# Kernel optimization log

Measured on AMD Instinct MI355X. Metric: run time of the kernel, lower is better.

Reference implementation:

```python
import jax, jax.numpy as jnp
import numpy as np

NUM_HEADS = 4
GN_GROUPS = 32
EPS = 1e-5


def setup_inputs() -> dict:
    key = jax.random.key(0)
    ks = jax.random.split(key, 6)
    B, C, H, W = 4, 256, 64, 64
    return {
        "x": jax.random.normal(ks[0], (B, C, H, W), dtype=jnp.float32),
        "gn_w": jnp.ones((C,), dtype=jnp.float32),
        "gn_b": jnp.zeros((C,), dtype=jnp.float32),
        "qkv_w": jax.random.normal(ks[1], (3 * C, C), dtype=jnp.float32) * 0.05,
        "qkv_b": jax.random.normal(ks[2], (3 * C,), dtype=jnp.float32) * 0.02,
        "proj_w": jax.random.normal(ks[3], (C, C), dtype=jnp.float32) * 0.05,
        "proj_b": jax.random.normal(ks[4], (C,), dtype=jnp.float32) * 0.02,
    }


def reference(x, gn_w, gn_b, qkv_w, qkv_b, proj_w, proj_b):
    b, c, h, w = x.shape
    L = h * w
    xf = x.reshape(b, c, L)

    # GroupNorm32: normalize over (channels_per_group, length) in float32
    xg = xf.reshape(b, GN_GROUPS, (c // GN_GROUPS) * L).astype(jnp.float32)
    mean = xg.mean(axis=-1, keepdims=True)
    var = xg.var(axis=-1, keepdims=True)
    xn = ((xg - mean) * jax.lax.rsqrt(var + EPS)).reshape(b, c, L).astype(x.dtype)
    xn = xn * gn_w[:, None] + gn_b[:, None]

    # 1x1 Conv1d == channel matmul: [3C, C] @ [b, C, L]
    qkv = jnp.einsum('oc,bcl->bol', qkv_w, xn) + qkv_b[:, None]

    # QKVAttentionLegacy
    ch = c // NUM_HEADS
    qkv_h = qkv.reshape(b * NUM_HEADS, 3 * ch, L)
    q, k, v = qkv_h[:, :ch], qkv_h[:, ch:2 * ch], qkv_h[:, 2 * ch:]
    scale = 1.0 / np.sqrt(np.sqrt(ch)).astype(np.float32)
    weight = jnp.einsum('bct,bcs->bts', q * scale, k * scale)  # [b*H, L, L]
    weight = jax.nn.softmax(weight.astype(jnp.float32), axis=-1).astype(qkv.dtype)
    a = jnp.einsum('bts,bcs->bct', weight, v).reshape(b, c, L)

    h_out = jnp.einsum('oc,bcl->bol', proj_w, a) + proj_b[:, None]
    return (xf + h_out).reshape(b, c, h, w)
```

## Files before the change

kernel.cpp:

```cpp
#include <hip/hip_runtime.h>
#include <math.h>

#define L 4096
#define C 256

typedef __attribute__((ext_vector_type(8))) short bf16x8;
typedef __attribute__((ext_vector_type(4))) short s16x4;
typedef __attribute__((ext_vector_type(4))) float f32x4;
typedef __attribute__((ext_vector_type(2))) unsigned int u32x2;
typedef __attribute__((ext_vector_type(4))) unsigned int u32x4;

#define MFMA16(a, b, c) __builtin_amdgcn_mfma_f32_16x16x32_bf16(a, b, c, 0, 0, 0)

static __device__ __forceinline__ short f2bf(float f) {
  union { float f; unsigned u; } x{f};
  unsigned r = (x.u + 0x7fffu + ((x.u >> 16) & 1u)) >> 16;
  return (short)r;
}
static __device__ __forceinline__ unsigned pack2(float a, float b) {
  return (unsigned)(unsigned short)f2bf(a) | ((unsigned)(unsigned short)f2bf(b) << 16);
}
static __device__ __forceinline__ unsigned ppack(float a, float b) {
  union { float f; unsigned u; } xa{a}, xb{b};
  return __builtin_amdgcn_perm(xb.u, xa.u, 0x07060302u);
}
static __device__ __forceinline__ float bflo(unsigned u) {
  union { unsigned u; float f; } x{u << 16};
  return x.f;
}
static __device__ __forceinline__ float bfhi(unsigned u) {
  union { unsigned u; float f; } x{u & 0xffff0000u};
  return x.f;
}
static __device__ __forceinline__ void gload_lds16(const void* g, void* l) {
  __builtin_amdgcn_global_load_lds(
      (const __attribute__((address_space(1))) unsigned int*)g,
      (__attribute__((address_space(3))) unsigned int*)l, 16, 0, 0);
}

__global__ __launch_bounds__(256) void prep(const float* __restrict__ x,
    float* __restrict__ gnp, short* __restrict__ xbf,
    const float* __restrict__ wa, const float* __restrict__ wb,
    short* __restrict__ da, short* __restrict__ db) {
  int blk = blockIdx.x;
  int tid = threadIdx.x;
  if (blk < 512) {
    size_t base = (size_t)blk * 8192;
    const f32x4* xp = (const f32x4*)(x + base);
    u32x2* xo = (u32x2*)(xbf + base);
    float s = 0.f, ss = 0.f;
    #pragma unroll
    for (int i = 0; i < 8; ++i) {
      f32x4 v = xp[i * 256 + tid];
      s  += v[0] + v[1] + v[2] + v[3];
      ss += v[0]*v[0] + v[1]*v[1] + v[2]*v[2] + v[3]*v[3];
      u32x2 o;
      o[0] = pack2(v[0], v[1]);
      o[1] = pack2(v[2], v[3]);
      xo[i * 256 + tid] = o;
    }
    __shared__ float rs[256], rss[256];
    rs[tid] = s; rss[tid] = ss;
    __syncthreads();
    for (int off = 128; off > 0; off >>= 1) {
      if (tid < off) { rs[tid] += rs[tid + off]; rss[tid] += rss[tid + off]; }
      __syncthreads();
    }
    if (tid == 0) {
      gnp[(size_t)blk * 2]     = rs[0];
      gnp[(size_t)blk * 2 + 1] = rss[0];
    }
  } else {
    int i = (blk - 512) * 256 + tid;
    if (i < 768 * C) da[i] = f2bf(wa[i]);
    else db[i - 768 * C] = f2bf(wb[i - 768 * C]);
  }
}

__global__ __launch_bounds__(256) void gn_apply(const short* __restrict__ xbf,
    const float* __restrict__ gw, const float* __restrict__ gb,
    const float* __restrict__ gnp, short* __restrict__ xnT) {
  int bg = blockIdx.y;
  int b = bg >> 5, g = bg & 31;
  int tid = threadIdx.x;
  const short* xg = xbf + (size_t)bg * 32768;

  float s  = gnp[(size_t)(bg*4)*2]   + gnp[(size_t)(bg*4+1)*2] +
             gnp[(size_t)(bg*4+2)*2] + gnp[(size_t)(bg*4+3)*2];
  float ss = gnp[(size_t)(bg*4)*2+1]   + gnp[(size_t)(bg*4+1)*2+1] +
             gnp[(size_t)(bg*4+2)*2+1] + gnp[(size_t)(bg*4+3)*2+1];
  float mean = s * (1.f / 32768.f);
  float var  = ss * (1.f / 32768.f) - mean * mean;
  float rstd = rsqrtf(var + 1e-5f);

  float scl[8], sft[8];
  #pragma unroll
  for (int c = 0; c < 8; ++c) {
    float wv = gw[g * 8 + c], bv = gb[g * 8 + c];
    scl[c] = rstd * wv;
    sft[c] = bv - mean * rstd * wv;
  }

  short* outb = xnT + (size_t)b * L * C + g * 8;
  int lb = blockIdx.x * 1024 + tid * 4;
  u32x2 raw[8];
  #pragma unroll
  for (int c = 0; c < 8; ++c)
    raw[c] = *(const u32x2*)(xg + (size_t)c * L + lb);
  #pragma unroll
  for (int j = 0; j < 4; ++j) {
    u32x4 ov;
    #pragma unroll
    for (int cp = 0; cp < 4; ++cp) {
      unsigned w0 = raw[2 * cp][j >> 1], w1 = raw[2 * cp + 1][j >> 1];
      float a = (j & 1) ? bfhi(w0) : bflo(w0);
      float bb = (j & 1) ? bfhi(w1) : bflo(w1);
      ov[cp] = pack2(a * scl[2 * cp] + sft[2 * cp],
                     bb * scl[2 * cp + 1] + sft[2 * cp + 1]);
    }
    *(u32x4*)(outb + (size_t)(lb + j) * C) = ov;
  }
}

__global__ __launch_bounds__(256) void qkv_mfma(const short* __restrict__ wq,
    const float* __restrict__ bias, const short* __restrict__ xnT,
    short* __restrict__ qT, short* __restrict__ kT, short* __restrict__ vB) {
  int tid = threadIdx.x;
  int wid = tid >> 6, lane = tid & 63, g = lane >> 4, lr = lane & 15;
  int oy = blockIdx.y;
  int o0 = oy * 64;
  int b  = blockIdx.z;
  int head = oy / 3, kind = oy % 3;
  int bh = b * 4 + head;
  int lw = blockIdx.x * 128 + wid * 32;
  const short* xb = xnT + (size_t)b * L * C;

  f32x4 acc[4][2];
  #pragma unroll
  for (int m = 0; m < 4; ++m)
    #pragma unroll
    for (int nt = 0; nt < 2; ++nt) acc[m][nt] = (f32x4)0.f;

  #pragma unroll 2
  for (int k0 = 0; k0 < C; k0 += 32) {
    bf16x8 af[4], bfr[2];
    #pragma unroll
    for (int m = 0; m < 4; ++m)
      af[m] = *(const bf16x8*)(wq + (size_t)(o0 + m * 16 + lr) * C + k0 + g * 8);
    #pragma unroll
    for (int nt = 0; nt < 2; ++nt)
      bfr[nt] = *(const bf16x8*)(xb + (size_t)(lw + nt * 16 + lr) * C + k0 + g * 8);
    #pragma unroll
    for (int m = 0; m < 4; ++m)
      #pragma unroll
      for (int nt = 0; nt < 2; ++nt)
        acc[m][nt] = MFMA16(af[m], bfr[nt], acc[m][nt]);
  }

  float sc = (kind == 0) ? 0.51014930f : (kind == 1) ? 0.35355339f : 1.0f;
  if (kind == 2) {
    #pragma unroll
    for (int m = 0; m < 4; ++m)
      #pragma unroll
      for (int nt = 0; nt < 2; ++nt)
        #pragma unroll
        for (int r = 0; r < 4; ++r) {
          int o = m * 16 + g * 4 + r;
          vB[((size_t)bh * 64 + o) * L + lw + nt * 16 + lr] =
              f2bf(acc[m][nt][r] + bias[o0 + o]);
        }
  } else {
    short* dst = (kind == 0 ? qT : kT);
    #pragma unroll
    for (int m = 0; m < 4; ++m)
      #pragma unroll
      for (int nt = 0; nt < 2; ++nt) {
        s16x4 pk;
        #pragma unroll
        for (int r = 0; r < 4; ++r)
          pk[r] = f2bf((acc[m][nt][r] + bias[o0 + m * 16 + g * 4 + r]) * sc);
        *(s16x4*)(dst + ((size_t)bh * L + lw + nt * 16 + lr) * 64 + m * 16 + g * 4) = pk;
      }
  }
}

__global__ __launch_bounds__(512) void attn_mfma(
    const short* __restrict__ qT, const short* __restrict__ kT,
    const short* __restrict__ vB, short* __restrict__ amatT) {
  int orig = blockIdx.x;
  int bid = (orig & 7) * 32 + (orig >> 3);
  int bh = bid >> 4, qb = bid & 15;
  int b = bh >> 2, h = bh & 3;
  int tid = threadIdx.x;
  int wid = tid >> 6, lane = tid & 63;
  int g = lane >> 4, lr = lane & 15;
  int tw = qb * 256 + wid * 32;
  int lx7 = lr & 7;
  int pswA = ((lr & 3) << 4) | ((lr >> 2) << 2);

  const short* qTh = qT + (size_t)bh * L * 64;
  const short* kTh = kT + (size_t)bh * L * 64;
  const short* vh  = vB + (size_t)bh * 64 * L;

  __shared__ short Kt[4][64 * 64];
  __shared__ short Vt[4][64 * 64];
  __shared__ short plds[8][32][64];

  bf16x8 qf[2][2];
  #pragma unroll
  for (int nt = 0; nt < 2; ++nt)
    #pragma unroll
    for (int ks = 0; ks < 2; ++ks)
      qf[nt][ks] = *(const bf16x8*)(qTh + (size_t)(tw + nt * 16 + lr) * 64 +
                                    ks * 32 + g * 8);

  bf16x8 ones;
  #pragma unroll
  for (int i = 0; i < 8; ++i) ones[i] = (short)0x3F80;

  f32x4 acc[4][2], acc_l[2];
  #pragma unroll
  for (int cm = 0; cm < 4; ++cm)
    #pragma unroll
    for (int nt = 0; nt < 2; ++nt) acc[cm][nt] = (f32x4)0.f;
  acc_l[0] = (f32x4)0.f; acc_l[1] = (f32x4)0.f;

  size_t koff, voff;
  int ldsc;
  {
    int r = tid >> 3, c16 = tid & 7;
    int cs = c16 ^ (r & 7);
    koff = (size_t)r * 64 + cs * 8;
    voff = (size_t)r * L + cs * 8;
    ldsc = wid * 512;
  }

  gload_lds16(kTh + koff, &Kt[0][ldsc]);
  gload_lds16(vh + voff, &Vt[0][ldsc]);
  gload_lds16(kTh + koff + (size_t)64 * 64, &Kt[1][ldsc]);
  gload_lds16(vh + voff + 64, &Vt[1][ldsc]);

  int sl = 0;
  #pragma unroll 1
  for (int s = 0; s < 32; ++s) {
    if (s < 31) {
      int nb = sl ^ 2;
      size_t t0 = (size_t)(2 * s + 2) * 64, t1 = (size_t)(2 * s + 3) * 64;
      gload_lds16(kTh + koff + t0 * 64, &Kt[nb][ldsc]);
      gload_lds16(vh + voff + t0, &Vt[nb][ldsc]);
      gload_lds16(kTh + koff + t1 * 64, &Kt[nb + 1][ldsc]);
      gload_lds16(vh + voff + t1, &Vt[nb + 1][ldsc]);
      asm volatile("s_waitcnt vmcnt(4)" ::: "memory");
    } else {
      asm volatile("s_waitcnt vmcnt(0)" ::: "memory");
    }
    __builtin_amdgcn_sched_barrier(0);
    __builtin_amdgcn_s_barrier();

    const short* Ka = &Kt[sl][0];     const short* Va = &Vt[sl][0];
    const short* Kb = &Kt[sl + 1][0]; const short* Vb = &Vt[sl + 1][0];

    f32x4 st0[4][2], st1[4][2];
    __builtin_amdgcn_s_setprio(1);
    #pragma unroll
    for (int sm = 0; sm < 4; ++sm) {
      int row = sm * 16 + lr;
      bf16x8 kf0 = *(const bf16x8*)&Ka[row * 64 + ((g ^ lx7)) * 8];
      bf16x8 kf1 = *(const bf16x8*)&Ka[row * 64 + (((4 + g) ^ lx7)) * 8];
      #pragma unroll
      for (int nt = 0; nt < 2; ++nt) {
        f32x4 cc = (f32x4)0.f;
        cc = MFMA16(kf0, qf[nt][0], cc);
        cc = MFMA16(kf1, qf[nt][1], cc);
        st0[sm][nt] = cc;
      }
    }
    __builtin_amdgcn_s_setprio(0);
    #pragma unroll
    for (int sm = 0; sm < 4; ++sm) {
      int row = sm * 16 + lr;
      bf16x8 kf0 = *(const bf16x8*)&Kb[row * 64 + ((g ^ lx7)) * 8];
      bf16x8 kf1 = *(const bf16x8*)&Kb[row * 64 + (((4 + g) ^ lx7)) * 8];
      #pragma unroll
      for (int nt = 0; nt < 2; ++nt) {
        f32x4 cc = (f32x4)0.f;
        cc = MFMA16(kf0, qf[nt][0], cc);
        cc = MFMA16(kf1, qf[nt][1], cc);
        st1[sm][nt] = cc;
        u32x2 w;
        w[0] = ppack(__builtin_amdgcn_exp2f(st0[sm][nt][0]),
                     __builtin_amdgcn_exp2f(st0[sm][nt][1]));
        w[1] = ppack(__builtin_amdgcn_exp2f(st0[sm][nt][2]),
                     __builtin_amdgcn_exp2f(st0[sm][nt][3]));
        *(u32x2*)&plds[wid][nt * 16 + lr][(sm * 16 + g * 4) ^ pswA] = w;
      }
    }
    bf16x8 pf0[2][2];
    #pragma unroll
    for (int nt = 0; nt < 2; ++nt)
      #pragma unroll
      for (int ks = 0; ks < 2; ++ks) {
        s16x4 pa = *(const s16x4*)&plds[wid][nt * 16 + lr][(ks * 32 + g * 8) ^ pswA];
        s16x4 pb = *(const s16x4*)&plds[wid][nt * 16 + lr][(ks * 32 + g * 8 + 4) ^ pswA];
        pf0[nt][ks] = __builtin_shufflevector(pa, pb, 0, 1, 2, 3, 4, 5, 6, 7);
      }
    #pragma unroll
    for (int nt = 0; nt < 2; ++nt) {
      acc_l[nt] = MFMA16(ones, pf0[nt][0], acc_l[nt]);
      acc_l[nt] = MFMA16(ones, pf0[nt][1], acc_l[nt]);
    }
    #pragma unroll
    for (int cm = 0; cm < 4; ++cm) {
      int row = cm * 16 + lr;
      bf16x8 vf0 = *(const bf16x8*)&Va[row * 64 + ((g ^ lx7)) * 8];
      bf16x8 vf1 = *(const bf16x8*)&Va[row * 64 + (((4 + g) ^ lx7)) * 8];
      #pragma unroll
      for (int nt = 0; nt < 2; ++nt) {
        acc[cm][nt] = MFMA16(vf0, pf0[nt][0], acc[cm][nt]);
        acc[cm][nt] = MFMA16(vf1, pf0[nt][1], acc[cm][nt]);
        u32x2 w;
        w[0] = ppack(__builtin_amdgcn_exp2f(st1[cm][nt][0]),
                     __builtin_amdgcn_exp2f(st1[cm][nt][1]));
        w[1] = ppack(__builtin_amdgcn_exp2f(st1[cm][nt][2]),
                     __builtin_amdgcn_exp2f(st1[cm][nt][3]));
        *(u32x2*)&plds[wid][nt * 16 + lr][(cm * 16 + g * 4) ^ pswA] = w;
      }
    }
    bf16x8 pf1[2][2];
    #pragma unroll
    for (int nt = 0; nt < 2; ++nt)
      #pragma unroll
      for (int ks = 0; ks < 2; ++ks) {
        s16x4 pa = *(const s16x4*)&plds[wid][nt * 16 + lr][(ks * 32 + g * 8) ^ pswA];
        s16x4 pb = *(const s16x4*)&plds[wid][nt * 16 + lr][(ks * 32 + g * 8 + 4) ^ pswA];
        pf1[nt][ks] = __builtin_shufflevector(pa, pb, 0, 1, 2, 3, 4, 5, 6, 7);
      }
    __builtin_amdgcn_s_setprio(1);
    #pragma unroll
    for (int nt = 0; nt < 2; ++nt) {
      acc_l[nt] = MFMA16(ones, pf1[nt][0], acc_l[nt]);
      acc_l[nt] = MFMA16(ones, pf1[nt][1], acc_l[nt]);
    }
    #pragma unroll
    for (int cm = 0; cm < 4; ++cm) {
      int row = cm * 16 + lr;
      bf16x8 vf0 = *(const bf16x8*)&Vb[row * 64 + ((g ^ lx7)) * 8];
      bf16x8 vf1 = *(const bf16x8*)&Vb[row * 64 + (((4 + g) ^ lx7)) * 8];
      #pragma unroll
      for (int nt = 0; nt < 2; ++nt) {
        acc[cm][nt] = MFMA16(vf0, pf1[nt][0], acc[cm][nt]);
        acc[cm][nt] = MFMA16(vf1, pf1[nt][1], acc[cm][nt]);
      }
    }
    __builtin_amdgcn_s_setprio(0);
    __builtin_amdgcn_s_barrier();
    sl ^= 2;
  }

  #pragma unroll
  for (int nt = 0; nt < 2; ++nt) {
    float inv = 1.f / acc_l[nt][0];
    #pragma unroll
    for (int cm = 0; cm < 4; ++cm) {
      s16x4 pk;
      #pragma unroll
      for (int r = 0; r < 4; ++r) pk[r] = f2bf(acc[cm][nt][r] * inv);
      *(s16x4*)(amatT + ((size_t)b * L + tw + nt * 16 + lr) * C + h * 64 +
                cm * 16 + g * 4) = pk;
    }
  }
}

__global__ __launch_bounds__(256) void proj_mfma(const short* __restrict__ pw,
    const float* __restrict__ bias, const short* __restrict__ amatT,
    const float* __restrict__ xres, float* __restrict__ out) {
  int tid = threadIdx.x;
  int wid = tid >> 6, lane = tid & 63, g = lane >> 4, lr = lane & 15;
  int o0 = blockIdx.y * 64;
  int b  = blockIdx.z;
  int lw = blockIdx.x * 128 + wid * 32;
  const short* ab = amatT + (size_t)b * L * C;

  f32x4 acc[4][2];
  #pragma unroll
  for (int m = 0; m < 4; ++m)
    #pragma unroll
    for (int nt = 0; nt < 2; ++nt) acc[m][nt] = (f32x4)0.f;

  #pragma unroll 2
  for (int k0 = 0; k0 < C; k0 += 32) {
    bf16x8 af[4], bfr[2];
    #pragma unroll
    for (int m = 0; m < 4; ++m)
      af[m] = *(const bf16x8*)(pw + (size_t)(o0 + m * 16 + lr) * C + k0 + g * 8);
    #pragma unroll
    for (int nt = 0; nt < 2; ++nt)
      bfr[nt] = *(const bf16x8*)(ab + (size_t)(lw + nt * 16 + lr) * C + k0 + g * 8);
    #pragma unroll
    for (int m = 0; m < 4; ++m)
      #pragma unroll
      for (int nt = 0; nt < 2; ++nt)
        acc[m][nt] = MFMA16(af[m], bfr[nt], acc[m][nt]);
  }

  #pragma unroll
  for (int m = 0; m < 4; ++m)
    #pragma unroll
    for (int nt = 0; nt < 2; ++nt)
      #pragma unroll
      for (int r = 0; r < 4; ++r) {
        int o = o0 + m * 16 + g * 4 + r;
        size_t idx = ((size_t)b * C + o) * L + lw + nt * 16 + lr;
        out[idx] = acc[m][nt][r] + bias[o] + xres[idx];
      }
}

extern "C" void kernel_launch(void* const* d_in, const int* in_sizes, int n_in,
                              void* d_out, int out_size, void* d_ws, size_t ws_size,
                              hipStream_t stream) {
  const float* x      = (const float*)d_in[0];
  const float* gn_w   = (const float*)d_in[1];
  const float* gn_b   = (const float*)d_in[2];
  const float* qkv_w  = (const float*)d_in[3];
  const float* qkv_b  = (const float*)d_in[4];
  const float* proj_w = (const float*)d_in[5];
  const float* proj_b = (const float*)d_in[6];
  float* out = (float*)d_out;

  short* xnT   = (short*)d_ws;
  short* qT    = xnT   + (size_t)4 * L * C;
  short* kT    = qT    + (size_t)16 * L * 64;
  short* vB    = kT    + (size_t)16 * L * 64;
  short* amatT = vB    + (size_t)16 * L * 64;
  short* xbf   = amatT + (size_t)4 * L * C;
  short* wqbf  = xbf   + (size_t)4 * C * L;
  short* pwbf  = wqbf  + (size_t)768 * C;
  float* gnp   = (float*)(pwbf + (size_t)C * C);

  prep<<<1536, 256, 0, stream>>>(x, gnp, xbf, qkv_w, proj_w, wqbf, pwbf);
  gn_apply<<<dim3(4, 128), 256, 0, stream>>>(xbf, gn_w, gn_b, gnp, xnT);
  qkv_mfma<<<dim3(32, 12, 4), 256, 0, stream>>>(wqbf, qkv_b, xnT, qT, kT, vB);
  attn_mfma<<<256, 512, 0, stream>>>(qT, kT, vB, amatT);
  proj_mfma<<<dim3(32, 4, 4), 256, 0, stream>>>(pwbf, proj_b, amatT, x, out);
}
```

Before: 149.7 us.

## Split attention KV range across two blocks and add a combine kernel

The attention kernel splits each query tile's key/value sequence into two halves handled by separate blocks (512 blocks instead of 256). Each block writes unnormalized bf16 partial outputs and row sums, and a new combine kernel adds them and normalizes. The P tile in LDS is halved and the exp/PV interleaving is restructured, with a launch-bounds occupancy hint added. This is meant to fill more CUs (256 blocks underfill the device), at the cost of an extra launch, a round trip of the partials through global memory, and extra bf16 rounding of the partials. There is no running max, so splitting the softmax needs no rescaling.

```diff
diff --git a/kernel.cpp b/kernel.cpp
--- a/kernel.cpp
+++ b/kernel.cpp
@@ -16,6 +16,10 @@
   union { float f; unsigned u; } x{f};
   unsigned r = (x.u + 0x7fffu + ((x.u >> 16) & 1u)) >> 16;
   return (short)r;
+}
+static __device__ __forceinline__ float bf2f(short s) {
+  union { unsigned u; float f; } x{((unsigned)(unsigned short)s) << 16};
+  return x.f;
 }
 static __device__ __forceinline__ unsigned pack2(float a, float b) {
   return (unsigned)(unsigned short)f2bf(a) | ((unsigned)(unsigned short)f2bf(b) << 16);
@@ -184,27 +188,30 @@
   }
 }
 
-__global__ __launch_bounds__(512) void attn_mfma(
+__global__ __launch_bounds__(512, 4) void attn_mfma(
     const short* __restrict__ qT, const short* __restrict__ kT,
-    const short* __restrict__ vB, short* __restrict__ amatT) {
+    const short* __restrict__ vB, short* __restrict__ part,
+    float* __restrict__ lsp) {
   int orig = blockIdx.x;
-  int bid = (orig & 7) * 32 + (orig >> 3);
-  int bh = bid >> 4, qb = bid & 15;
+  int bid = (orig & 7) * 64 + (orig >> 3);
+  int bh = bid >> 5, qb = (bid >> 1) & 15, kv = bid & 1;
   int b = bh >> 2, h = bh & 3;
+  (void)b; (void)h;
   int tid = threadIdx.x;
   int wid = tid >> 6, lane = tid & 63;
   int g = lane >> 4, lr = lane & 15;
   int tw = qb * 256 + wid * 32;
   int lx7 = lr & 7;
-  int pswA = ((lr & 3) << 4) | ((lr >> 2) << 2);
+  int psw = ((lr & 3) << 4) | ((lr >> 2) << 2);
 
   const short* qTh = qT + (size_t)bh * L * 64;
   const short* kTh = kT + (size_t)bh * L * 64;
   const short* vh  = vB + (size_t)bh * 64 * L;
+  size_t kvb = (size_t)kv * 2048;
 
   __shared__ short Kt[4][64 * 64];
   __shared__ short Vt[4][64 * 64];
-  __shared__ short plds[8][32][64];
+  __shared__ short plds[8][16][64];
 
   bf16x8 qf[2][2];
   #pragma unroll
@@ -235,21 +242,23 @@
     ldsc = wid * 512;
   }
 
-  gload_lds16(kTh + koff, &Kt[0][ldsc]);
-  gload_lds16(vh + voff, &Vt[0][ldsc]);
-  gload_lds16(kTh + koff + (size_t)64 * 64, &Kt[1][ldsc]);
-  gload_lds16(vh + voff + 64, &Vt[1][ldsc]);
+  #define STAGE(buf, s0v)                                              \
+    {                                                                  \
+      gload_lds16(kTh + koff + (size_t)(s0v) * 64, &Kt[buf][ldsc]);    \
+      gload_lds16(vh + voff + (size_t)(s0v), &Vt[buf][ldsc]);          \
+    }
+
+  STAGE(0, kvb);
+  STAGE(1, kvb + 64);
 
   int sl = 0;
   #pragma unroll 1
-  for (int s = 0; s < 32; ++s) {
-    if (s < 31) {
+  for (int s = 0; s < 16; ++s) {
+    if (s < 15) {
       int nb = sl ^ 2;
-      size_t t0 = (size_t)(2 * s + 2) * 64, t1 = (size_t)(2 * s + 3) * 64;
-      gload_lds16(kTh + koff + t0 * 64, &Kt[nb][ldsc]);
-      gload_lds16(vh + voff + t0, &Vt[nb][ldsc]);
-      gload_lds16(kTh + koff + t1 * 64, &Kt[nb + 1][ldsc]);
-      gload_lds16(vh + voff + t1, &Vt[nb + 1][ldsc]);
+      size_t t0 = kvb + (size_t)(2 * s + 2) * 64, t1 = kvb + (size_t)(2 * s + 3) * 64;
+      STAGE(nb, t0);
+      STAGE(nb + 1, t1);
       asm volatile("s_waitcnt vmcnt(4)" ::: "memory");
     } else {
       asm volatile("s_waitcnt vmcnt(0)" ::: "memory");
@@ -276,6 +285,7 @@
       }
     }
     __builtin_amdgcn_s_setprio(0);
+    u32x2 pwA[4][2];
     #pragma unroll
     for (int sm = 0; sm < 4; ++sm) {
       int row = sm * 16 + lr;
@@ -292,83 +302,110 @@
                      __builtin_amdgcn_exp2f(st0[sm][nt][1]));
         w[1] = ppack(__builtin_amdgcn_exp2f(st0[sm][nt][2]),
                      __builtin_amdgcn_exp2f(st0[sm][nt][3]));
-        *(u32x2*)&plds[wid][nt * 16 + lr][(sm * 16 + g * 4) ^ pswA] = w;
-      }
-    }
-    bf16x8 pf0[2][2];
-    #pragma unroll
-    for (int nt = 0; nt < 2; ++nt)
+        pwA[sm][nt] = w;
+      }
+    }
+    u32x2 pwB[4][2];
+    #pragma unroll
+    for (int sm = 0; sm < 4; ++sm)
+      #pragma unroll
+      for (int nt = 0; nt < 2; ++nt) {
+        u32x2 w;
+        w[0] = ppack(__builtin_amdgcn_exp2f(st1[sm][nt][0]),
+                     __builtin_amdgcn_exp2f(st1[sm][nt][1]));
+        w[1] = ppack(__builtin_amdgcn_exp2f(st1[sm][nt][2]),
+                     __builtin_amdgcn_exp2f(st1[sm][nt][3]));
+        pwB[sm][nt] = w;
+      }
+    #pragma unroll
+    for (int nt = 0; nt < 2; ++nt) {
+      #pragma unroll
+      for (int sm = 0; sm < 4; ++sm)
+        *(u32x2*)&plds[wid][lr][(sm * 16 + g * 4) ^ psw] = pwA[sm][nt];
+      bf16x8 pf[2];
       #pragma unroll
       for (int ks = 0; ks < 2; ++ks) {
-        s16x4 pa = *(const s16x4*)&plds[wid][nt * 16 + lr][(ks * 32 + g * 8) ^ pswA];
-        s16x4 pb = *(const s16x4*)&plds[wid][nt * 16 + lr][(ks * 32 + g * 8 + 4) ^ pswA];
-        pf0[nt][ks] = __builtin_shufflevector(pa, pb, 0, 1, 2, 3, 4, 5, 6, 7);
-      }
+        s16x4 pa = *(const s16x4*)&plds[wid][lr][(ks * 32 + g * 8) ^ psw];
+        s16x4 pb = *(const s16x4*)&plds[wid][lr][(ks * 32 + g * 8 + 4) ^ psw];
+        pf[ks] = __builtin_shufflevector(pa, pb, 0, 1, 2, 3, 4, 5, 6, 7);
+      }
+      __builtin_amdgcn_s_setprio(1);
+      acc_l[nt] = MFMA16(ones, pf[0], acc_l[nt]);
+      acc_l[nt] = MFMA16(ones, pf[1], acc_l[nt]);
+      #pragma unroll
+      for (int cm = 0; cm < 4; ++cm) {
+        int row = cm * 16 + lr;
+        bf16x8 vf0 = *(const bf16x8*)&Va[row * 64 + ((g ^ lx7)) * 8];
+        bf16x8 vf1 = *(const bf16x8*)&Va[row * 64 + (((4 + g) ^ lx7)) * 8];
+        acc[cm][nt] = MFMA16(vf0, pf[0], acc[cm][nt]);
+        acc[cm][nt] = MFMA16(vf1, pf[1], acc[cm][nt]);
+      }
+      __builtin_amdgcn_s_setprio(0);
+    }
     #pragma unroll
     for (int nt = 0; nt < 2; ++nt) {
-      acc_l[nt] = MFMA16(ones, pf0[nt][0], acc_l[nt]);
-      acc_l[nt] = MFMA16(ones, pf0[nt][1], acc_l[nt]);
-    }
-    #pragma unroll
-    for (int cm = 0; cm < 4; ++cm) {
-      int row = cm * 16 + lr;
-      bf16x8 vf0 = *(const bf16x8*)&Va[row * 64 + ((g ^ lx7)) * 8];
-      bf16x8 vf1 = *(const bf16x8*)&Va[row * 64 + (((4 + g) ^ lx7)) * 8];
-      #pragma unroll
-      for (int nt = 0; nt < 2; ++nt) {
-        acc[cm][nt] = MFMA16(vf0, pf0[nt][0], acc[cm][nt]);
-        acc[cm][nt] = MFMA16(vf1, pf0[nt][1], acc[cm][nt]);
-        u32x2 w;
-        w[0] = ppack(__builtin_amdgcn_exp2f(st1[cm][nt][0]),
-                     __builtin_amdgcn_exp2f(st1[cm][nt][1]));
-        w[1] = ppack(__builtin_amdgcn_exp2f(st1[cm][nt][2]),
-                     __builtin_amdgcn_exp2f(st1[cm][nt][3]));
-        *(u32x2*)&plds[wid][nt * 16 + lr][(cm * 16 + g * 4) ^ pswA] = w;
-      }
-    }
-    bf16x8 pf1[2][2];
-    #pragma unroll
-    for (int nt = 0; nt < 2; ++nt)
+      #pragma unroll
+      for (int sm = 0; sm < 4; ++sm)
+        *(u32x2*)&plds[wid][lr][(sm * 16 + g * 4) ^ psw] = pwB[sm][nt];
+      bf16x8 pf[2];
       #pragma unroll
       for (int ks = 0; ks < 2; ++ks) {
-        s16x4 pa = *(const s16x4*)&plds[wid][nt * 16 + lr][(ks * 32 + g * 8) ^ pswA];
-        s16x4 pb = *(const s16x4*)&plds[wid][nt * 16 + lr][(ks * 32 + g * 8 + 4) ^ pswA];
-        pf1[nt][ks] = __builtin_shufflevector(pa, pb, 0, 1, 2, 3, 4, 5, 6, 7);
-      }
-    __builtin_amdgcn_s_setprio(1);
-    #pragma unroll
-    for (int nt = 0; nt < 2; ++nt) {
-      acc_l[nt] = MFMA16(ones, pf1[nt][0], acc_l[nt]);
-      acc_l[nt] = MFMA16(ones, pf1[nt][1], acc_l[nt]);
-    }
-    #pragma unroll
-    for (int cm = 0; cm < 4; ++cm) {
-      int row = cm * 16 + lr;
-      bf16x8 vf0 = *(const bf16x8*)&Vb[row * 64 + ((g ^ lx7)) * 8];
-      bf16x8 vf1 = *(const bf16x8*)&Vb[row * 64 + (((4 + g) ^ lx7)) * 8];
-      #pragma unroll
-      for (int nt = 0; nt < 2; ++nt) {
-        acc[cm][nt] = MFMA16(vf0, pf1[nt][0], acc[cm][nt]);
-        acc[cm][nt] = MFMA16(vf1, pf1[nt][1], acc[cm][nt]);
-      }
-    }
-    __builtin_amdgcn_s_setprio(0);
+        s16x4 pa = *(const s16x4*)&plds[wid][lr][(ks * 32 + g * 8) ^ psw];
+        s16x4 pb = *(const s16x4*)&plds[wid][lr][(ks * 32 + g * 8 + 4) ^ psw];
+        pf[ks] = __builtin_shufflevector(pa, pb, 0, 1, 2, 3, 4, 5, 6, 7);
+      }
+      __builtin_amdgcn_s_setprio(1);
+      acc_l[nt] = MFMA16(ones, pf[0], acc_l[nt]);
+      acc_l[nt] = MFMA16(ones, pf[1], acc_l[nt]);
+      #pragma unroll
+      for (int cm = 0; cm < 4; ++cm) {
+        int row = cm * 16 + lr;
+        bf16x8 vf0 = *(const bf16x8*)&Vb[row * 64 + ((g ^ lx7)) * 8];
+        bf16x8 vf1 = *(const bf16x8*)&Vb[row * 64 + (((4 + g) ^ lx7)) * 8];
+        acc[cm][nt] = MFMA16(vf0, pf[0], acc[cm][nt]);
+        acc[cm][nt] = MFMA16(vf1, pf[1], acc[cm][nt]);
+      }
+      __builtin_amdgcn_s_setprio(0);
+    }
     __builtin_amdgcn_s_barrier();
     sl ^= 2;
   }
 
+  short* pb = part + (((size_t)(kv * 16 + bh)) * L + tw) * 64;
   #pragma unroll
   for (int nt = 0; nt < 2; ++nt) {
-    float inv = 1.f / acc_l[nt][0];
     #pragma unroll
     for (int cm = 0; cm < 4; ++cm) {
       s16x4 pk;
       #pragma unroll
-      for (int r = 0; r < 4; ++r) pk[r] = f2bf(acc[cm][nt][r] * inv);
-      *(s16x4*)(amatT + ((size_t)b * L + tw + nt * 16 + lr) * C + h * 64 +
-                cm * 16 + g * 4) = pk;
-    }
-  }
+      for (int r = 0; r < 4; ++r) pk[r] = f2bf(acc[cm][nt][r]);
+      *(s16x4*)(pb + (size_t)(nt * 16 + lr) * 64 + cm * 16 + g * 4) = pk;
+    }
+    if (g == 0)
+      lsp[((size_t)(kv * 16 + bh)) * L + tw + nt * 16 + lr] = acc_l[nt][0];
+  }
+  #undef STAGE
+}
+
+__global__ __launch_bounds__(256) void combine(const short* __restrict__ part,
+    const float* __restrict__ lsp, short* __restrict__ amatT) {
+  int idx = blockIdx.x * 256 + threadIdx.x;
+  int bh = idx >> 16;
+  int rem = idx & 65535;
+  int q = rem >> 4, d4 = rem & 15;
+  int b = bh >> 2, h = bh & 3;
+  size_t o0 = ((size_t)bh * L + q) * 64 + d4 * 4;
+  s16x4 p0 = *(const s16x4*)(part + o0);
+  s16x4 p1 = *(const s16x4*)(part + (size_t)16 * L * 64 + o0);
+  float l0 = lsp[(size_t)bh * L + q];
+  float l1 = lsp[(size_t)16 * L * 16 / 16 * 16 + (size_t)bh * L + q - (size_t)bh * L + (size_t)(16 + bh) * L + q - q - (size_t)16 * L * 0];
+  l1 = lsp[((size_t)(16 + bh)) * L + q];
+  float inv = 1.f / (l0 + l1);
+  s16x4 pk;
+  #pragma unroll
+  for (int r = 0; r < 4; ++r)
+    pk[r] = f2bf((bf2f(p0[r]) + bf2f(p1[r])) * inv);
+  *(s16x4*)(amatT + ((size_t)b * L + q) * C + h * 64 + d4 * 4) = pk;
 }
 
 __global__ __launch_bounds__(256) void proj_mfma(const short* __restrict__ pw,
@@ -433,13 +470,16 @@
   short* vB    = kT    + (size_t)16 * L * 64;
   short* amatT = vB    + (size_t)16 * L * 64;
   short* xbf   = amatT + (size_t)4 * L * C;
-  short* wqbf  = xbf   + (size_t)4 * C * L;
+  short* part  = xbf   + (size_t)4 * C * L;
+  short* wqbf  = part  + (size_t)2 * 16 * L * 64;
   short* pwbf  = wqbf  + (size_t)768 * C;
   float* gnp   = (float*)(pwbf + (size_t)C * C);
+  float* lsp   = gnp + 1024;
 
   prep<<<1536, 256, 0, stream>>>(x, gnp, xbf, qkv_w, proj_w, wqbf, pwbf);
   gn_apply<<<dim3(4, 128), 256, 0, stream>>>(xbf, gn_w, gn_b, gnp, xnT);
   qkv_mfma<<<dim3(32, 12, 4), 256, 0, stream>>>(wqbf, qkv_b, xnT, qT, kT, vB);
-  attn_mfma<<<256, 512, 0, stream>>>(qT, kT, vB, amatT);
+  attn_mfma<<<512, 512, 0, stream>>>(qT, kT, vB, part, lsp);
+  combine<<<4096, 256, 0, stream>>>(part, lsp, amatT);
   proj_mfma<<<dim3(32, 4, 4), 256, 0, stream>>>(pwbf, proj_b, amatT, x, out);
 }
```

Result: slower. 157.6 us (+5.3%).

## Stage GN transpose and QKV epilogue stores through LDS for coalesced writes

Applied to the files above, without the earlier changes.

The GroupNorm apply kernel is restructured so each block handles 64 spatial positions across all 256 channels. It computes per-group scale and shift in shared memory and transposes through an LDS tile, so global stores become full-row vector writes. The QKV GEMM epilogue also buffers its outputs in LDS before writing contiguous 16-byte chunks, replacing scattered 2-byte and 8-byte stores. This targets uncoalesced global writes, at the cost of extra LDS traffic, possible bank conflicts from the strided tile writes, and added barriers.

```diff
diff --git a/kernel.cpp b/kernel.cpp
--- a/kernel.cpp
+++ b/kernel.cpp
@@ -80,45 +80,55 @@
 __global__ __launch_bounds__(256) void gn_apply(const short* __restrict__ xbf,
     const float* __restrict__ gw, const float* __restrict__ gb,
     const float* __restrict__ gnp, short* __restrict__ xnT) {
-  int bg = blockIdx.y;
-  int b = bg >> 5, g = bg & 31;
+  int b = blockIdx.y;
+  int l0 = blockIdx.x * 64;
   int tid = threadIdx.x;
-  const short* xg = xbf + (size_t)bg * 32768;
-
-  float s  = gnp[(size_t)(bg*4)*2]   + gnp[(size_t)(bg*4+1)*2] +
-             gnp[(size_t)(bg*4+2)*2] + gnp[(size_t)(bg*4+3)*2];
-  float ss = gnp[(size_t)(bg*4)*2+1]   + gnp[(size_t)(bg*4+1)*2+1] +
-             gnp[(size_t)(bg*4+2)*2+1] + gnp[(size_t)(bg*4+3)*2+1];
-  float mean = s * (1.f / 32768.f);
-  float var  = ss * (1.f / 32768.f) - mean * mean;
-  float rstd = rsqrtf(var + 1e-5f);
-
-  float scl[8], sft[8];
-  #pragma unroll
-  for (int c = 0; c < 8; ++c) {
-    float wv = gw[g * 8 + c], bv = gb[g * 8 + c];
-    scl[c] = rstd * wv;
-    sft[c] = bv - mean * rstd * wv;
-  }
-
-  short* outb = xnT + (size_t)b * L * C + g * 8;
-  int lb = blockIdx.x * 1024 + tid * 4;
-  u32x2 raw[8];
-  #pragma unroll
-  for (int c = 0; c < 8; ++c)
-    raw[c] = *(const u32x2*)(xg + (size_t)c * L + lb);
-  #pragma unroll
-  for (int j = 0; j < 4; ++j) {
-    u32x4 ov;
-    #pragma unroll
-    for (int cp = 0; cp < 4; ++cp) {
-      unsigned w0 = raw[2 * cp][j >> 1], w1 = raw[2 * cp + 1][j >> 1];
-      float a = (j & 1) ? bfhi(w0) : bflo(w0);
-      float bb = (j & 1) ? bfhi(w1) : bflo(w1);
-      ov[cp] = pack2(a * scl[2 * cp] + sft[2 * cp],
-                     bb * scl[2 * cp + 1] + sft[2 * cp + 1]);
-    }
-    *(u32x4*)(outb + (size_t)(lb + j) * C) = ov;
+
+  __shared__ float scl[256], sft[256];
+  __shared__ short tile[64][264];
+
+  if (tid < 32) {
+    int g = tid;
+    int bg = b * 32 + g;
+    float s = 0.f, ss = 0.f;
+    #pragma unroll
+    for (int q = 0; q < 4; ++q) {
+      s  += gnp[(size_t)(bg * 4 + q) * 2];
+      ss += gnp[(size_t)(bg * 4 + q) * 2 + 1];
+    }
+    float mean = s * (1.f / 32768.f);
+    float var  = ss * (1.f / 32768.f) - mean * mean;
+    float rstd = rsqrtf(var + 1e-5f);
+    #pragma unroll
+    for (int c = 0; c < 8; ++c) {
+      float wv = gw[g * 8 + c], bv = gb[g * 8 + c];
+      scl[g * 8 + c] = rstd * wv;
+      sft[g * 8 + c] = bv - mean * rstd * wv;
+    }
+  }
+  __syncthreads();
+
+  const short* xb = xbf + (size_t)b * C * L;
+  #pragma unroll
+  for (int p = 0; p < 16; ++p) {
+    int c = p * 16 + (tid >> 4);
+    int ll = (tid & 15) * 4;
+    u32x2 r = *(const u32x2*)(xb + (size_t)c * L + l0 + ll);
+    float sc = scl[c], sf = sft[c];
+    tile[ll][c]     = f2bf(bflo(r[0]) * sc + sf);
+    tile[ll + 1][c] = f2bf(bfhi(r[0]) * sc + sf);
+    tile[ll + 2][c] = f2bf(bflo(r[1]) * sc + sf);
+    tile[ll + 3][c] = f2bf(bfhi(r[1]) * sc + sf);
+  }
+  __syncthreads();
+
+  short* ob = xnT + ((size_t)b * L + l0) * C;
+  int lrow = tid >> 2, ch = tid & 3;
+  #pragma unroll
+  for (int k = 0; k < 8; ++k) {
+    int c0 = ch * 8 + k * 32;
+    u32x4 v = *(const u32x4*)&tile[lrow][c0];
+    *(u32x4*)(ob + (size_t)lrow * C + c0) = v;
   }
 }
 
@@ -133,7 +143,10 @@
   int head = oy / 3, kind = oy % 3;
   int bh = b * 4 + head;
   int lw = blockIdx.x * 128 + wid * 32;
+  int lwb = blockIdx.x * 128;
   const short* xb = xnT + (size_t)b * L * C;
+
+  __shared__ short obuf[128 * 72];
 
   f32x4 acc[4][2];
   #pragma unroll
@@ -162,25 +175,44 @@
     #pragma unroll
     for (int m = 0; m < 4; ++m)
       #pragma unroll
-      for (int nt = 0; nt < 2; ++nt)
+      for (int nt = 0; nt < 2; ++nt) {
+        int l = wid * 32 + nt * 16 + lr;
         #pragma unroll
         for (int r = 0; r < 4; ++r) {
           int o = m * 16 + g * 4 + r;
-          vB[((size_t)bh * 64 + o) * L + lw + nt * 16 + lr] =
-              f2bf(acc[m][nt][r] + bias[o0 + o]);
+          obuf[o * 136 + l] = f2bf(acc[m][nt][r] + bias[o0 + o]);
         }
+      }
+    __syncthreads();
+    int o = tid >> 2, ch = tid & 3;
+    #pragma unroll
+    for (int k = 0; k < 4; ++k) {
+      int c0 = ch * 8 + k * 32;
+      u32x4 v = *(const u32x4*)&obuf[o * 136 + c0];
+      *(u32x4*)(vB + ((size_t)bh * 64 + o) * L + lwb + c0) = v;
+    }
   } else {
     short* dst = (kind == 0 ? qT : kT);
     #pragma unroll
     for (int m = 0; m < 4; ++m)
       #pragma unroll
       for (int nt = 0; nt < 2; ++nt) {
+        int l = wid * 32 + nt * 16 + lr;
         s16x4 pk;
         #pragma unroll
         for (int r = 0; r < 4; ++r)
           pk[r] = f2bf((acc[m][nt][r] + bias[o0 + m * 16 + g * 4 + r]) * sc);
-        *(s16x4*)(dst + ((size_t)bh * L + lw + nt * 16 + lr) * 64 + m * 16 + g * 4) = pk;
-      }
+        *(s16x4*)&obuf[l * 72 + m * 16 + g * 4] = pk;
+      }
+    __syncthreads();
+    short* db2 = dst + ((size_t)bh * L + lwb) * 64;
+    #pragma unroll
+    for (int p = 0; p < 4; ++p) {
+      int idx = p * 2048 + tid * 8;
+      int l = idx >> 6, c = idx & 63;
+      u32x4 v = *(const u32x4*)&obuf[l * 72 + c];
+      *(u32x4*)(db2 + idx) = v;
+    }
   }
 }
 
@@ -438,7 +470,7 @@
   float* gnp   = (float*)(pwbf + (size_t)C * C);
 
   prep<<<1536, 256, 0, stream>>>(x, gnp, xbf, qkv_w, proj_w, wqbf, pwbf);
-  gn_apply<<<dim3(4, 128), 256, 0, stream>>>(xbf, gn_w, gn_b, gnp, xnT);
+  gn_apply<<<dim3(64, 4), 256, 0, stream>>>(xbf, gn_w, gn_b, gnp, xnT);
   qkv_mfma<<<dim3(32, 12, 4), 256, 0, stream>>>(wqbf, qkv_b, xnT, qT, kT, vB);
   attn_mfma<<<256, 512, 0, stream>>>(qT, kT, vB, amatT);
   proj_mfma<<<dim3(32, 4, 4), 256, 0, stream>>>(pwbf, proj_b, amatT, x, out);
```

Result: faster. 145.4 us, median of 2 (-2.8%).
